# Kernel tuning notes

Measured on AMD Instinct MI355X. Metric: run time of the kernel, lower is better.

Reference implementation:

```python
import jax, jax.numpy as jnp
import numpy as np

H = 768
NH = 12
HD = H // NH
FF = 3072
EPS = 1e-12
SCALE = 1.0 / (HD ** 0.5)


def _ln(x, g, b):
    m = jnp.mean(x, axis=-1, keepdims=True)
    v = jnp.mean((x - m) ** 2, axis=-1, keepdims=True)
    return (x - m) * jax.lax.rsqrt(v + EPS) * g + b


def setup_inputs() -> dict:
    key = jax.random.key(0)
    ks = jax.random.split(key, 16)
    B, Q, S, T = 8, 64, 48, 128
    s = 0.02
    return {
        "q": jax.random.normal(ks[0], (B, Q, H), jnp.float32),
        "k": jax.random.normal(ks[1], (B, S, T, H), jnp.float32),
        "mask": jax.random.randint(ks[2], (B, S, T), 0, 2, jnp.int32),
        "Wq": jax.random.normal(ks[3], (H, H), jnp.float32) * s,
        "Wkv": jax.random.normal(ks[4], (H, H), jnp.float32) * s,
        "Wo": jax.random.normal(ks[5], (H, H), jnp.float32) * s,
        "bo": jnp.zeros((H,), jnp.float32),
        "ln1_g": jnp.ones((H,), jnp.float32),
        "ln1_b": jnp.zeros((H,), jnp.float32),
        "W1": jax.random.normal(ks[6], (H, FF), jnp.float32) * s,
        "b1": jnp.zeros((FF,), jnp.float32),
        "W2": jax.random.normal(ks[7], (FF, H), jnp.float32) * s,
        "b2": jnp.zeros((H,), jnp.float32),
        "ln2_g": jnp.ones((H,), jnp.float32),
        "ln2_b": jnp.zeros((H,), jnp.float32),
    }


def reference(q, k, mask, Wq, Wkv, Wo, bo, ln1_g, ln1_b, W1, b1, W2, b2, ln2_g, ln2_b):
    B, Q, _ = q.shape
    _, S, T, _ = k.shape
    # projections (no bias)
    qp = (q @ Wq).reshape(B, Q, NH, HD)            # [b,q,h,d]
    kv = (k @ Wkv).reshape(B, S, T, NH, HD)        # [b,s,t,h,d]
    # broadcast-query grouped attention: softmax only over token dim t
    scores = jnp.einsum('bqhd,bsthd->bhqst', qp, kv) * SCALE
    scores = scores + mask.astype(scores.dtype)[:, None, None, :, :] * -10000.0
    alpha = jax.nn.softmax(scores, axis=-1)        # dropout is identity in eval
    res = jnp.einsum('bhqst,bsthd->bqshd', alpha, kv).reshape(B, Q, S, H)
    # BertSelfOutput with zero residual (residual=False)
    attn_out = _ln(res @ Wo + bo, ln1_g, ln1_b)    # [b,q,s,H]
    # FFN
    ffn = jax.nn.gelu(attn_out @ W1 + b1, approximate=False) @ W2 + b2
    return _ln(attn_out + ffn, ln2_g, ln2_b)
```

## Files before the change

### kernel.cpp

```cpp
#include <hip/hip_runtime.h>
#include <hip/hip_bf16.h>
#include <math.h>

#define B_ 8
#define Q_ 64
#define S_ 48
#define T_ 128
#define H_ 768
#define NH_ 12
#define HD_ 64
#define FF_ 3072

typedef float f32x4 __attribute__((ext_vector_type(4)));
typedef short s16x8 __attribute__((ext_vector_type(8)));
typedef short s16x4 __attribute__((ext_vector_type(4)));

__device__ __forceinline__ float ldT(const float* p, size_t i) { return p[i]; }
__device__ __forceinline__ float ldT(const __hip_bfloat16* p, size_t i) { return __bfloat162float(p[i]); }
__device__ __forceinline__ void stT(float* p, size_t i, float v) { p[i] = v; }
__device__ __forceinline__ void stT(__hip_bfloat16* p, size_t i, float v) { p[i] = __float2bfloat16(v); }

__device__ __forceinline__ short f2bf(float f) {
  __hip_bfloat16 h = __float2bfloat16(f);
  return *reinterpret_cast<short*>(&h);
}

__device__ __forceinline__ float gelu_f(float x) {
  return 0.5f * x * (1.0f + erff(x * 0.70710678118654752f));
}

__device__ __forceinline__ void gld_lds16(const void* g, void* l) {
  __builtin_amdgcn_global_load_lds(
      (const __attribute__((address_space(1))) void*)g,
      (__attribute__((address_space(3))) void*)l, 16, 0, 0);
}

__device__ __forceinline__ int swz_off(int row, int kc) {
  return row * 64 + ((kc ^ ((row >> 1) & 3)) << 4);
}

template<typename OT, bool BIAS, bool GELU>
__global__ __launch_bounds__(256) void gemm_mfma(
    const __hip_bfloat16* __restrict__ A,
    const __hip_bfloat16* __restrict__ BT,
    const float* __restrict__ bias, OT* __restrict__ C,
    int N, int K, int nbx)
{
  __shared__ char sm[3][16384];

  int wg = blockIdx.x;
  const int q8 = gridDim.x >> 3;
  wg = (wg & 7) * q8 + (wg >> 3);
  const int bm = wg / nbx;
  const int bn = wg % nbx;
  const int m0 = bm * 128, n0 = bn * 128;

  const int tid = threadIdx.x;
  const int lane = tid & 63;
  const int wid = tid >> 6;
  const int wr = wid >> 1, wc = wid & 1;

  const int nt = K >> 5;

  auto stage = [&](int buf, int kt) {
    const int k0 = kt << 5;
    const __hip_bfloat16* Ab = A + (size_t)m0 * K + k0;
    const __hip_bfloat16* Bb = BT + (size_t)n0 * K + k0;
    char* smA = sm[buf];
    char* smB = sm[buf] + 8192;
    #pragma unroll
    for (int r = 0; r < 2; ++r) {
      const int c = tid + r * 256;
      const int row = c >> 2, slot = c & 3;
      const int kc = slot ^ ((row >> 1) & 3);
      gld_lds16(Ab + (size_t)row * K + kc * 8, smA + c * 16);
      gld_lds16(Bb + (size_t)row * K + kc * 8, smB + c * 16);
    }
  };

  f32x4 acc[4][4] = {};
  stage(0, 0);
  if (nt > 1) stage(1, 1);

  int cur = 0;
  for (int kt = 0; kt < nt; ++kt) {
    if (kt + 1 < nt) asm volatile("s_waitcnt vmcnt(4)" ::: "memory");
    else             asm volatile("s_waitcnt vmcnt(0)" ::: "memory");
    __builtin_amdgcn_s_barrier();
    asm volatile("" ::: "memory");

    const char* smA = sm[cur];
    const char* smB = sm[cur] + 8192;
    const int kc = lane >> 4, rl = lane & 15;
    s16x8 af[4], bf[4];
    #pragma unroll
    for (int m = 0; m < 4; ++m)
      af[m] = *(const s16x8*)(smA + swz_off(wr * 64 + m * 16 + rl, kc));
    #pragma unroll
    for (int n = 0; n < 4; ++n)
      bf[n] = *(const s16x8*)(smB + swz_off(wc * 64 + n * 16 + rl, kc));

    int nb = cur + 2; if (nb >= 3) nb -= 3;
    if (kt + 2 < nt) stage(nb, kt + 2);

    #pragma unroll
    for (int m = 0; m < 4; ++m)
      #pragma unroll
      for (int n = 0; n < 4; ++n)
        acc[m][n] = __builtin_amdgcn_mfma_f32_16x16x32_bf16(af[m], bf[n], acc[m][n], 0, 0, 0);

    ++cur; if (cur == 3) cur = 0;
  }

  const int colb = n0 + wc * 64 + (lane & 15);
  const int rowb = m0 + wr * 64 + (lane >> 4) * 4;
  float bv[4];
  #pragma unroll
  for (int n = 0; n < 4; ++n) bv[n] = BIAS ? bias[colb + n * 16] : 0.0f;
  #pragma unroll
  for (int m = 0; m < 4; ++m) {
    #pragma unroll
    for (int r = 0; r < 4; ++r) {
      const int row = rowb + m * 16 + r;
      #pragma unroll
      for (int n = 0; n < 4; ++n) {
        float v = acc[m][n][r] + bv[n];
        if (GELU) v = gelu_f(v);
        stT(C, (size_t)row * N + colb + n * 16, v);
      }
    }
  }
}

template<typename OT>
__global__ __launch_bounds__(256) void gemm64(
    const float* __restrict__ A, const float* __restrict__ W,
    OT* __restrict__ C, int M, int N, int K)
{
  __shared__ float As[16][65];
  __shared__ float Ws[16][65];
  const int tid = threadIdx.x;
  const int m0 = blockIdx.y * 64;
  const int n0 = blockIdx.x * 64;
  const int tx = (tid & 15) * 4;
  const int ty = (tid >> 4) * 4;
  float acc[4][4] = {};

  for (int k0 = 0; k0 < K; k0 += 16) {
    #pragma unroll
    for (int r = 0; r < 4; ++r) {
      int idx = tid + r * 256;
      int mm = idx >> 4, kk = idx & 15;
      As[kk][mm] = A[(size_t)(m0 + mm) * K + (k0 + kk)];
    }
    #pragma unroll
    for (int r = 0; r < 4; ++r) {
      int idx = tid + r * 256;
      int kk = idx >> 6, nn = idx & 63;
      Ws[kk][nn] = W[(size_t)(k0 + kk) * N + (n0 + nn)];
    }
    __syncthreads();
    #pragma unroll
    for (int kk = 0; kk < 16; ++kk) {
      float a[4], b[4];
      #pragma unroll
      for (int i = 0; i < 4; ++i) a[i] = As[kk][ty + i];
      #pragma unroll
      for (int j = 0; j < 4; ++j) b[j] = Ws[kk][tx + j];
      #pragma unroll
      for (int i = 0; i < 4; ++i)
        #pragma unroll
        for (int j = 0; j < 4; ++j) acc[i][j] += a[i] * b[j];
    }
    __syncthreads();
  }
  #pragma unroll
  for (int i = 0; i < 4; ++i)
    #pragma unroll
    for (int j = 0; j < 4; ++j)
      stT(C, (size_t)(m0 + ty + i) * N + (n0 + tx + j), acc[i][j]);
}

__global__ __launch_bounds__(256) void transpose_cast(
    const float* __restrict__ W, __hip_bfloat16* __restrict__ WT, int K, int N)
{
  __shared__ float t[32][33];
  const int n0 = blockIdx.x * 32, k0 = blockIdx.y * 32;
  const int x = threadIdx.x & 31, y4 = (threadIdx.x >> 5) * 4;
  #pragma unroll
  for (int i = 0; i < 4; ++i)
    t[y4 + i][x] = W[(size_t)(k0 + y4 + i) * N + n0 + x];
  __syncthreads();
  #pragma unroll
  for (int i = 0; i < 4; ++i)
    WT[(size_t)(n0 + y4 + i) * K + k0 + x] = __float2bfloat16(t[x][y4 + i]);
}

__global__ __launch_bounds__(256) void cast_f32_bf16(
    const float* __restrict__ x, __hip_bfloat16* __restrict__ y, size_t n4)
{
  const size_t i = (size_t)blockIdx.x * 256 + threadIdx.x;
  if (i >= n4) return;
  const float4 v = ((const float4*)x)[i];
  __hip_bfloat16 o[4] = { __float2bfloat16(v.x), __float2bfloat16(v.y),
                          __float2bfloat16(v.z), __float2bfloat16(v.w) };
  *(ushort4*)(y + i * 4) = *(ushort4*)o;
}

__global__ __launch_bounds__(256) void attn_mfma(
    const __hip_bfloat16* __restrict__ qp,
    const __hip_bfloat16* __restrict__ kvp,
    const int* __restrict__ mask,
    __hip_bfloat16* __restrict__ res)
{
  const int s = blockIdx.x, h = blockIdx.y, b = blockIdx.z;
  __shared__ __align__(16) char lds[66048];
  char* Ks = lds;
  char* VT = lds + 16384;
  char* SC = lds + 32768;
  float* mv = (float*)(lds + 65536);

  const int tid = threadIdx.x;
  const int lane = tid & 63;
  const int wid = tid >> 6;
  const int wr = wid >> 1, wc = wid & 1;
  const int kcg = lane >> 4, rl = lane & 15;

  if (tid < 128) mv[tid] = (float)mask[((size_t)b * S_ + s) * T_ + tid] * -10000.0f;

  {
    const __hip_bfloat16* qb = qp + ((size_t)b * Q_) * H_ + h * HD_;
    #pragma unroll
    for (int r = 0; r < 2; ++r) {
      const int c = tid + r * 256;
      const int qq = c >> 3, sc = c & 7;
      const int kc8 = sc ^ (qq & 7);
      gld_lds16(qb + (size_t)qq * H_ + kc8 * 8, SC + c * 16);
    }
  }
  {
    const int kc8 = tid & 7, tg = tid >> 3;
    const int t0 = tg * 4;
    const __hip_bfloat16* kb = kvp + (((size_t)b * S_ + s) * T_) * H_ + h * HD_ + kc8 * 8;
    s16x8 r0 = *(const s16x8*)(kb + (size_t)(t0 + 0) * H_);
    s16x8 r1 = *(const s16x8*)(kb + (size_t)(t0 + 1) * H_);
    s16x8 r2 = *(const s16x8*)(kb + (size_t)(t0 + 2) * H_);
    s16x8 r3 = *(const s16x8*)(kb + (size_t)(t0 + 3) * H_);
    *(s16x8*)(Ks + (t0 + 0) * 128 + ((kc8 ^ ((t0 + 0) & 7)) << 4)) = r0;
    *(s16x8*)(Ks + (t0 + 1) * 128 + ((kc8 ^ ((t0 + 1) & 7)) << 4)) = r1;
    *(s16x8*)(Ks + (t0 + 2) * 128 + ((kc8 ^ ((t0 + 2) & 7)) << 4)) = r2;
    *(s16x8*)(Ks + (t0 + 3) * 128 + ((kc8 ^ ((t0 + 3) & 7)) << 4)) = r3;
    const int tc = tg >> 1;
    const int toff = (tg & 1) * 8;
    #pragma unroll
    for (int j = 0; j < 8; ++j) {
      s16x4 v4 = { r0[j], r1[j], r2[j], r3[j] };
      const int d = kc8 * 8 + j;
      *(s16x4*)(VT + d * 256 + ((tc ^ (d & 15)) << 4) + toff) = v4;
    }
  }
  __syncthreads();

  f32x4 acc[2][4] = {};
  {
    s16x8 af[2][2], bf[2][4];
    #pragma unroll
    for (int kk = 0; kk < 2; ++kk) {
      #pragma unroll
      for (int m = 0; m < 2; ++m) {
        const int q = wr * 32 + m * 16 + rl;
        const int kc8 = kk * 4 + kcg;
        af[kk][m] = *(const s16x8*)(SC + q * 128 + ((kc8 ^ (q & 7)) << 4));
      }
      #pragma unroll
      for (int n = 0; n < 4; ++n) {
        const int t = wc * 64 + n * 16 + rl;
        const int kc8 = kk * 4 + kcg;
        bf[kk][n] = *(const s16x8*)(Ks + t * 128 + ((kc8 ^ (t & 7)) << 4));
      }
    }
    #pragma unroll
    for (int kk = 0; kk < 2; ++kk)
      #pragma unroll
      for (int m = 0; m < 2; ++m)
        #pragma unroll
        for (int n = 0; n < 4; ++n)
          acc[m][n] = __builtin_amdgcn_mfma_f32_16x16x32_bf16(af[kk][m], bf[kk][n], acc[m][n], 0, 0, 0);
  }
  __syncthreads();

  #pragma unroll
  for (int m = 0; m < 2; ++m)
    #pragma unroll
    for (int n = 0; n < 4; ++n)
      #pragma unroll
      for (int r = 0; r < 4; ++r) {
        const int q = wr * 32 + m * 16 + (lane >> 4) * 4 + r;
        const int t = wc * 64 + n * 16 + rl;
        const int tc32 = t >> 2;
        *(float*)(SC + q * 512 + ((tc32 ^ (q & 31)) << 4) + (t & 3) * 4) =
            acc[m][n][r] * 0.125f + mv[t];
      }
  __syncthreads();

  {
    const int q = tid >> 2, quarter = tid & 3;
    float vals[32];
    #pragma unroll
    for (int j = 0; j < 8; ++j) {
      const int tc32 = quarter * 8 + j;
      const f32x4 c = *(const f32x4*)(SC + q * 512 + ((tc32 ^ (q & 31)) << 4));
      vals[j * 4 + 0] = c[0]; vals[j * 4 + 1] = c[1];
      vals[j * 4 + 2] = c[2]; vals[j * 4 + 3] = c[3];
    }
    float mx = -1e30f;
    #pragma unroll
    for (int i = 0; i < 32; ++i) mx = fmaxf(mx, vals[i]);
    mx = fmaxf(mx, __shfl_xor(mx, 1, 64));
    mx = fmaxf(mx, __shfl_xor(mx, 2, 64));
    float sum = 0.0f;
    #pragma unroll
    for (int i = 0; i < 32; ++i) { vals[i] = expf(vals[i] - mx); sum += vals[i]; }
    sum += __shfl_xor(sum, 1, 64);
    sum += __shfl_xor(sum, 2, 64);
    const float inv = 1.0f / sum;
    #pragma unroll
    for (int jj = 0; jj < 4; ++jj) {
      const int tcp = quarter * 4 + jj;
      s16x8 pk;
      #pragma unroll
      for (int i = 0; i < 8; ++i) pk[i] = f2bf(vals[jj * 8 + i] * inv);
      *(s16x8*)(SC + q * 512 + ((tcp ^ (q & 15)) << 4)) = pk;
    }
  }
  __syncthreads();

  f32x4 oacc[2][2] = {};
  #pragma unroll
  for (int kt = 0; kt < 4; ++kt) {
    s16x8 pa[2], vb[2];
    #pragma unroll
    for (int m = 0; m < 2; ++m) {
      const int q = wr * 32 + m * 16 + rl;
      const int tcp = kt * 4 + kcg;
      pa[m] = *(const s16x8*)(SC + q * 512 + ((tcp ^ (q & 15)) << 4));
    }
    #pragma unroll
    for (int n = 0; n < 2; ++n) {
      const int d = wc * 32 + n * 16 + rl;
      const int tc = kt * 4 + kcg;
      vb[n] = *(const s16x8*)(VT + d * 256 + ((tc ^ (d & 15)) << 4));
    }
    #pragma unroll
    for (int m = 0; m < 2; ++m)
      #pragma unroll
      for (int n = 0; n < 2; ++n)
        oacc[m][n] = __builtin_amdgcn_mfma_f32_16x16x32_bf16(pa[m], vb[n], oacc[m][n], 0, 0, 0);
  }
  #pragma unroll
  for (int m = 0; m < 2; ++m)
    #pragma unroll
    for (int n = 0; n < 2; ++n)
      #pragma unroll
      for (int r = 0; r < 4; ++r) {
        const int q = wr * 32 + m * 16 + (lane >> 4) * 4 + r;
        const int d = wc * 32 + n * 16 + rl;
        res[(((size_t)b * Q_ + q) * S_ + s) * H_ + h * HD_ + d] =
            __float2bfloat16(oacc[m][n][r]);
      }
}

template<bool ADD, typename IT, typename OT>
__global__ __launch_bounds__(256) void ln_kernel(
    const IT* __restrict__ X, const IT* __restrict__ X2,
    const float* __restrict__ g, const float* __restrict__ bta,
    OT* __restrict__ Y)
{
  const size_t row = blockIdx.x;
  const int tid = threadIdx.x;
  float v[3];
  #pragma unroll
  for (int i = 0; i < 3; ++i) {
    int c = tid + i * 256;
    v[i] = ldT(X, row * H_ + c);
    if (ADD) v[i] += ldT(X2, row * H_ + c);
  }
  float sum = v[0] + v[1] + v[2];
  #pragma unroll
  for (int off = 32; off > 0; off >>= 1) sum += __shfl_down(sum, off, 64);
  __shared__ float red[8];
  const int w = tid >> 6;
  if ((tid & 63) == 0) red[w] = sum;
  __syncthreads();
  const float mean = (red[0] + red[1] + red[2] + red[3]) * (1.0f / 768.0f);
  float vs = 0.0f;
  #pragma unroll
  for (int i = 0; i < 3; ++i) { v[i] -= mean; vs += v[i] * v[i]; }
  #pragma unroll
  for (int off = 32; off > 0; off >>= 1) vs += __shfl_down(vs, off, 64);
  if ((tid & 63) == 0) red[4 + w] = vs;
  __syncthreads();
  const float rstd = rsqrtf((red[4] + red[5] + red[6] + red[7]) * (1.0f / 768.0f) + 1e-12f);
  #pragma unroll
  for (int i = 0; i < 3; ++i) {
    int c = tid + i * 256;
    stT(Y, row * H_ + c, v[i] * rstd * g[c] + bta[c]);
  }
}

extern "C" void kernel_launch(void* const* d_in, const int* in_sizes, int n_in,
                              void* d_out, int out_size, void* d_ws, size_t ws_size,
                              hipStream_t stream) {
  const float* q    = (const float*)d_in[0];
  const float* k    = (const float*)d_in[1];
  const int*   mask = (const int*)d_in[2];
  const float* Wq   = (const float*)d_in[3];
  const float* Wkv  = (const float*)d_in[4];
  const float* Wo   = (const float*)d_in[5];
  const float* bo   = (const float*)d_in[6];
  const float* ln1g = (const float*)d_in[7];
  const float* ln1b = (const float*)d_in[8];
  const float* W1   = (const float*)d_in[9];
  const float* b1   = (const float*)d_in[10];
  const float* W2   = (const float*)d_in[11];
  const float* b2   = (const float*)d_in[12];
  const float* ln2g = (const float*)d_in[13];
  const float* ln2b = (const float*)d_in[14];
  float* out = (float*)d_out;

  const int MROWS = B_ * Q_ * S_;
  const int KVROWS = B_ * S_ * T_;

  char* ws = (char*)d_ws;
  __hip_bfloat16* kbf  = (__hip_bfloat16*)ws;
  __hip_bfloat16* kvp  = (__hip_bfloat16*)(ws + 75497472);
  __hip_bfloat16* ffn1 = (__hip_bfloat16*)ws;
  __hip_bfloat16* ares = (__hip_bfloat16*)(ws + 150994944);
  __hip_bfloat16* ffn2 = ares;
  __hip_bfloat16* aln  = (__hip_bfloat16*)(ws + 188743680);
  __hip_bfloat16* qp   = (__hip_bfloat16*)(ws + 226492416);
  __hip_bfloat16* WkvT = (__hip_bfloat16*)(ws + 228065280);
  __hip_bfloat16* WoT  = (__hip_bfloat16*)(ws + 229244928);
  __hip_bfloat16* W1T  = (__hip_bfloat16*)(ws + 230424576);
  __hip_bfloat16* W2T  = (__hip_bfloat16*)(ws + 235143168);

  dim3 blk(256);

  transpose_cast<<<dim3(24, 24), blk, 0, stream>>>(Wkv, WkvT, H_, H_);
  transpose_cast<<<dim3(24, 24), blk, 0, stream>>>(Wo, WoT, H_, H_);
  transpose_cast<<<dim3(96, 24), blk, 0, stream>>>(W1, W1T, H_, FF_);
  transpose_cast<<<dim3(24, 96), blk, 0, stream>>>(W2, W2T, FF_, H_);
  cast_f32_bf16<<<dim3((KVROWS * H_ / 4 + 255) / 256), blk, 0, stream>>>(
      k, kbf, (size_t)KVROWS * H_ / 4);

  gemm64<__hip_bfloat16><<<dim3(H_ / 64, 512 / 64), blk, 0, stream>>>(
      q, Wq, qp, 512, H_, H_);
  gemm_mfma<__hip_bfloat16, false, false>
      <<<dim3((KVROWS / 128) * (H_ / 128)), blk, 0, stream>>>(
      kbf, WkvT, nullptr, kvp, H_, H_, H_ / 128);
  attn_mfma<<<dim3(S_, NH_, B_), blk, 0, stream>>>(qp, kvp, mask, ares);
  gemm_mfma<float, true, false>
      <<<dim3((MROWS / 128) * (H_ / 128)), blk, 0, stream>>>(
      ares, WoT, bo, out, H_, H_, H_ / 128);
  ln_kernel<false, float, __hip_bfloat16><<<MROWS, blk, 0, stream>>>(
      out, nullptr, ln1g, ln1b, aln);
  gemm_mfma<__hip_bfloat16, true, true>
      <<<dim3((MROWS / 128) * (FF_ / 128)), blk, 0, stream>>>(
      aln, W1T, b1, ffn1, FF_, H_, FF_ / 128);
  gemm_mfma<__hip_bfloat16, true, false>
      <<<dim3((MROWS / 128) * (H_ / 128)), blk, 0, stream>>>(
      ffn1, W2T, b2, ffn2, H_, FF_, H_ / 128);
  ln_kernel<true, __hip_bfloat16, float><<<MROWS, blk, 0, stream>>>(
      aln, ffn2, ln2g, ln2b, out);
}
```

Measured before the change: 658.6 us.

## Group GEMM tiles per XCD for L2 reuse, precompute load pointers, bf16 Wo output

Changes the GEMM block-to-tile mapping so each XCD owns a contiguous band of M rows and walks them in groups of GB row-tiles across all N columns. The aim is better L2 reuse of A and B tiles within an XCD. Global-load addresses are now computed once and advanced by pointer increments instead of being recomputed every k-step. The Wo projection now writes bf16 pre-LayerNorm activations to scratch instead of fp32 into the output buffer, which halves that intermediate's traffic at some cost in precision before LN1.

```diff
diff --git a/kernel.cpp b/kernel.cpp
--- a/kernel.cpp
+++ b/kernel.cpp
@@ -44,15 +44,19 @@
     const __hip_bfloat16* __restrict__ A,
     const __hip_bfloat16* __restrict__ BT,
     const float* __restrict__ bias, OT* __restrict__ C,
-    int N, int K, int nbx)
+    int N, int K, int nbx, int GB)
 {
   __shared__ char sm[3][16384];
 
-  int wg = blockIdx.x;
-  const int q8 = gridDim.x >> 3;
-  wg = (wg & 7) * q8 + (wg >> 3);
-  const int bm = wg / nbx;
-  const int bn = wg % nbx;
+  const int cpx = gridDim.x >> 3;
+  const int xcd = blockIdx.x & 7;
+  const int ci  = blockIdx.x >> 3;
+  const int gsz = GB * nbx;
+  const int g   = ci / gsz;
+  const int r2  = ci - g * gsz;
+  const int bn  = r2 / GB;
+  const int bi  = r2 - bn * GB;
+  const int bm  = xcd * (cpx / nbx) + g * GB + bi;
   const int m0 = bm * 128, n0 = bn * 128;
 
   const int tid = threadIdx.x;
@@ -62,25 +66,29 @@
 
   const int nt = K >> 5;
 
-  auto stage = [&](int buf, int kt) {
-    const int k0 = kt << 5;
-    const __hip_bfloat16* Ab = A + (size_t)m0 * K + k0;
-    const __hip_bfloat16* Bb = BT + (size_t)n0 * K + k0;
+  const __hip_bfloat16* pA[2];
+  const __hip_bfloat16* pB[2];
+  #pragma unroll
+  for (int r = 0; r < 2; ++r) {
+    const int c = tid + r * 256, row = c >> 2, slot = c & 3;
+    const int kc = slot ^ ((row >> 1) & 3);
+    pA[r] = A + (size_t)(m0 + row) * K + kc * 8;
+    pB[r] = BT + (size_t)(n0 + row) * K + kc * 8;
+  }
+  auto stage = [&](int buf) {
     char* smA = sm[buf];
     char* smB = sm[buf] + 8192;
     #pragma unroll
     for (int r = 0; r < 2; ++r) {
-      const int c = tid + r * 256;
-      const int row = c >> 2, slot = c & 3;
-      const int kc = slot ^ ((row >> 1) & 3);
-      gld_lds16(Ab + (size_t)row * K + kc * 8, smA + c * 16);
-      gld_lds16(Bb + (size_t)row * K + kc * 8, smB + c * 16);
+      const int c16 = (tid + r * 256) * 16;
+      gld_lds16(pA[r], smA + c16); pA[r] += 32;
+      gld_lds16(pB[r], smB + c16); pB[r] += 32;
     }
   };
 
   f32x4 acc[4][4] = {};
-  stage(0, 0);
-  if (nt > 1) stage(1, 1);
+  stage(0);
+  if (nt > 1) stage(1);
 
   int cur = 0;
   for (int kt = 0; kt < nt; ++kt) {
@@ -101,7 +109,7 @@
       bf[n] = *(const s16x8*)(smB + swz_off(wc * 64 + n * 16 + rl, kc));
 
     int nb = cur + 2; if (nb >= 3) nb -= 3;
-    if (kt + 2 < nt) stage(nb, kt + 2);
+    if (kt + 2 < nt) stage(nb);
 
     #pragma unroll
     for (int m = 0; m < 4; ++m)
@@ -433,6 +441,7 @@
 
   char* ws = (char*)d_ws;
   __hip_bfloat16* kbf  = (__hip_bfloat16*)ws;
+  __hip_bfloat16* apre = (__hip_bfloat16*)ws;
   __hip_bfloat16* kvp  = (__hip_bfloat16*)(ws + 75497472);
   __hip_bfloat16* ffn1 = (__hip_bfloat16*)ws;
   __hip_bfloat16* ares = (__hip_bfloat16*)(ws + 150994944);
@@ -457,19 +466,19 @@
       q, Wq, qp, 512, H_, H_);
   gemm_mfma<__hip_bfloat16, false, false>
       <<<dim3((KVROWS / 128) * (H_ / 128)), blk, 0, stream>>>(
-      kbf, WkvT, nullptr, kvp, H_, H_, H_ / 128);
+      kbf, WkvT, nullptr, kvp, H_, H_, H_ / 128, 6);
   attn_mfma<<<dim3(S_, NH_, B_), blk, 0, stream>>>(qp, kvp, mask, ares);
-  gemm_mfma<float, true, false>
+  gemm_mfma<__hip_bfloat16, true, false>
       <<<dim3((MROWS / 128) * (H_ / 128)), blk, 0, stream>>>(
-      ares, WoT, bo, out, H_, H_, H_ / 128);
-  ln_kernel<false, float, __hip_bfloat16><<<MROWS, blk, 0, stream>>>(
-      out, nullptr, ln1g, ln1b, aln);
+      ares, WoT, bo, apre, H_, H_, H_ / 128, 6);
+  ln_kernel<false, __hip_bfloat16, __hip_bfloat16><<<MROWS, blk, 0, stream>>>(
+      apre, nullptr, ln1g, ln1b, aln);
   gemm_mfma<__hip_bfloat16, true, true>
       <<<dim3((MROWS / 128) * (FF_ / 128)), blk, 0, stream>>>(
-      aln, W1T, b1, ffn1, FF_, H_, FF_ / 128);
+      aln, W1T, b1, ffn1, FF_, H_, FF_ / 128, 6);
   gemm_mfma<__hip_bfloat16, true, false>
       <<<dim3((MROWS / 128) * (H_ / 128)), blk, 0, stream>>>(
-      ffn1, W2T, b2, ffn2, H_, FF_, H_ / 128);
+      ffn1, W2T, b2, ffn2, H_, FF_, H_ / 128, 4);
   ln_kernel<true, __hip_bfloat16, float><<<MROWS, blk, 0, stream>>>(
       aln, ffn2, ln2g, ln2b, out);
 }
```

Result: faster. 629.6 us (-4.4%).
